# Kernel optimization log

Measured on AMD Instinct MI355X. Metric: run time of the kernel, lower is better.

Reference implementation:

```python
import jax, jax.numpy as jnp
import numpy as np

N_NODES = 50000
N_EDGES = 800000
IN_C, HID_C, OUT_C = 64, 128, 40


def setup_inputs() -> dict:
    key = jax.random.key(0)
    ks = jax.random.split(key, 8)
    x = jax.random.normal(ks[0], (N_NODES, IN_C), dtype=jnp.float32)
    edge_index = jax.random.randint(ks[1], (2, N_EDGES), 0, N_NODES, dtype=jnp.int64)
    def lin(k, fan_in, fan_out):
        # torch Linear default init: U(-1/sqrt(fan_in), 1/sqrt(fan_in))
        bound = 1.0 / np.sqrt(fan_in)
        kw, kb = jax.random.split(k)
        w = jax.random.uniform(kw, (fan_in, fan_out), minval=-bound, maxval=bound, dtype=jnp.float32)
        b = jax.random.uniform(kb, (fan_out,), minval=-bound, maxval=bound, dtype=jnp.float32)
        return w, b
    w1a, b1a = lin(ks[2], IN_C, HID_C)
    w1b, b1b = lin(ks[3], HID_C, HID_C)
    w2a, b2a = lin(ks[4], HID_C, HID_C)
    w2b, b2b = lin(ks[5], HID_C, OUT_C)
    return {
        'x': x, 'edge_index': edge_index,
        'w1a': w1a, 'b1a': b1a, 'w1b': w1b, 'b1b': b1b, 'eps1': jnp.float32(0.0),
        'w2a': w2a, 'b2a': b2a, 'w2b': w2b, 'b2b': b2b, 'eps2': jnp.float32(0.0),
    }


def _gin_conv(x, src, dst, eps, wa, ba, wb, bb):
    # aggregate: sum of neighbor (source) features at each destination node
    agg = jax.ops.segment_sum(x[src], dst, num_segments=N_NODES)  # [N, d]
    h = (1.0 + eps) * x + agg
    h = jax.nn.relu(h @ wa + ba)
    return h @ wb + bb


def reference(x, edge_index, w1a, b1a, w1b, b1b, eps1, w2a, b2a, w2b, b2b, eps2):
    src, dst = edge_index[0], edge_index[1]
    h = _gin_conv(x, src, dst, eps1, w1a, b1a, w1b, b1b)
    h = jax.nn.relu(h)
    # F.dropout(training=False) -> identity at inference
    h = _gin_conv(h, src, dst, eps2, w2a, b2a, w2b, b2b)
    return jax.nn.log_softmax(h, axis=1)
```

## Files before the change

### kernel.cpp

```cpp
#include <hip/hip_runtime.h>
#include <math.h>

#define N_NODES 50000
#define N_EDGES 800000

typedef __attribute__((ext_vector_type(4))) _Float16 half4;
typedef __attribute__((ext_vector_type(8))) _Float16 half8;
typedef __attribute__((ext_vector_type(4))) float f32x4;

__global__ __launch_bounds__(256) void convert_zero(const float4* __restrict__ in,
    half4* __restrict__ out, int* __restrict__ zbase)
{
    int i = blockIdx.x * 256 + threadIdx.x;
    if (i < 450000) zbase[i] = 0;
    if (i < 800000) {
        float4 v = in[i];
        half4 h;
        h[0] = (_Float16)v.x; h[1] = (_Float16)v.y;
        h[2] = (_Float16)v.z; h[3] = (_Float16)v.w;
        out[i] = h;
    }
}

__global__ __launch_bounds__(256) void scatter_ell(const int* __restrict__ src,
    const int* __restrict__ dst, int* __restrict__ cursor8, int* __restrict__ ovcur,
    unsigned short* __restrict__ ellp, unsigned short* __restrict__ ovell)
{
    int g = blockIdx.x & 7;
    int el = (blockIdx.x >> 3) * 256 + threadIdx.x;
    if (el >= 100000) return;
    int e = g * 100000 + el;
    int d = dst[e];
    unsigned short s = (unsigned short)src[e];
    int slot = atomicAdd(&cursor8[g * 50000 + d], 1);
    if (slot < 8) ellp[(size_t)(g * 50000 + d) * 8 + slot] = s;
    else {
        int o = atomicAdd(&ovcur[d], 1);
        if (o < 16) ovell[d * 16 + o] = s;
    }
}

__global__ __launch_bounds__(256) void compact_ell(const int* __restrict__ cursor8,
    const int* __restrict__ ovcur, const unsigned short* __restrict__ ellp,
    const unsigned short* __restrict__ ovell,
    unsigned short* __restrict__ ell, int* __restrict__ deg)
{
    __shared__ unsigned short buf[4][80];
    const int w = threadIdx.x >> 6, lane = threadIdx.x & 63;
    const int node = blockIdx.x * 4 + w;
    const int g = lane >> 3, sl = lane & 7;
    int cg = min(cursor8[g * 50000 + node], 8);
    bool valid = sl < cg;
    unsigned short v = ellp[(size_t)(g * 50000 + node) * 8 + sl];
    unsigned long long mask = __ballot(valid);
    int total = __popcll(mask);
    int pos = __popcll(mask & ((1ULL << lane) - 1ULL));
    if (valid) buf[w][pos] = v;
    int ov = min(ovcur[node], 16);
    if (lane < ov) buf[w][total + lane] = ovell[node * 16 + lane];
    __syncthreads();
    int tot = min(total + ov, 64);
    ell[((size_t)node << 6) + lane] = (lane < tot) ? buf[w][lane] : (unsigned short)0;
    if (lane == 0) deg[node] = tot;
}

__global__ __launch_bounds__(256) void gather64(const half4* __restrict__ rows,
    const unsigned short* __restrict__ ell, const int* __restrict__ deg,
    const float* __restrict__ epsp, half4* __restrict__ z)
{
    const float eps = 1.0f + epsp[0];
    const int lane = threadIdx.x & 63;
    const int q = lane & 15, p = lane >> 4;
    const int wid = blockIdx.x * 4 + (threadIdx.x >> 6);
    const int wstep = gridDim.x * 4;

    for (int node = wid; node < N_NODES; node += wstep) {
        const int cnt = min(deg[node], 64);
        int eidx = (lane < cnt) ? ell[((size_t)node << 6) + lane] : 0;
        float4 acc = make_float4(0.f, 0.f, 0.f, 0.f);
        for (int i = 0; i < cnt; i += 16) {
            int s0 = __shfl(eidx, i + p);
            int s1 = __shfl(eidx, i + 4 + p);
            int s2 = __shfl(eidx, i + 8 + p);
            int s3 = __shfl(eidx, i + 12 + p);
            half4 v0 = rows[s0 * 16 + q];
            half4 v1 = rows[s1 * 16 + q];
            half4 v2 = rows[s2 * 16 + q];
            half4 v3 = rows[s3 * 16 + q];
            bool k0 = (i + p) < cnt, k1 = (i + 4 + p) < cnt;
            bool k2 = (i + 8 + p) < cnt, k3 = (i + 12 + p) < cnt;
            acc.x += (k0?(float)v0[0]:0.f)+(k1?(float)v1[0]:0.f)+(k2?(float)v2[0]:0.f)+(k3?(float)v3[0]:0.f);
            acc.y += (k0?(float)v0[1]:0.f)+(k1?(float)v1[1]:0.f)+(k2?(float)v2[1]:0.f)+(k3?(float)v3[1]:0.f);
            acc.z += (k0?(float)v0[2]:0.f)+(k1?(float)v1[2]:0.f)+(k2?(float)v2[2]:0.f)+(k3?(float)v3[2]:0.f);
            acc.w += (k0?(float)v0[3]:0.f)+(k1?(float)v1[3]:0.f)+(k2?(float)v2[3]:0.f)+(k3?(float)v3[3]:0.f);
        }
        acc.x += __shfl_xor(acc.x, 16); acc.y += __shfl_xor(acc.y, 16);
        acc.z += __shfl_xor(acc.z, 16); acc.w += __shfl_xor(acc.w, 16);
        acc.x += __shfl_xor(acc.x, 32); acc.y += __shfl_xor(acc.y, 32);
        acc.z += __shfl_xor(acc.z, 32); acc.w += __shfl_xor(acc.w, 32);
        if (p == 0) {
            half4 sv = rows[node * 16 + q];
            half4 o;
            o[0] = (_Float16)fmaf(eps, (float)sv[0], acc.x);
            o[1] = (_Float16)fmaf(eps, (float)sv[1], acc.y);
            o[2] = (_Float16)fmaf(eps, (float)sv[2], acc.z);
            o[3] = (_Float16)fmaf(eps, (float)sv[3], acc.w);
            z[node * 16 + q] = o;
        }
    }
}

__global__ __launch_bounds__(256) void gather128(const half4* __restrict__ rows,
    const unsigned short* __restrict__ ell, const int* __restrict__ deg,
    const float* __restrict__ epsp, half4* __restrict__ z)
{
    const float eps = 1.0f + epsp[0];
    const int lane = threadIdx.x & 63;
    const int q = lane & 31, p = lane >> 5;
    const int wid = blockIdx.x * 4 + (threadIdx.x >> 6);
    const int wstep = gridDim.x * 4;

    for (int node = wid; node < N_NODES; node += wstep) {
        const int cnt = min(deg[node], 64);
        int eidx = (lane < cnt) ? ell[((size_t)node << 6) + lane] : 0;
        float4 acc = make_float4(0.f, 0.f, 0.f, 0.f);
        for (int i = 0; i < cnt; i += 8) {
            int s0 = __shfl(eidx, i + p);
            int s1 = __shfl(eidx, i + 2 + p);
            int s2 = __shfl(eidx, i + 4 + p);
            int s3 = __shfl(eidx, i + 6 + p);
            half4 v0 = rows[s0 * 32 + q];
            half4 v1 = rows[s1 * 32 + q];
            half4 v2 = rows[s2 * 32 + q];
            half4 v3 = rows[s3 * 32 + q];
            bool k0 = (i + p) < cnt, k1 = (i + 2 + p) < cnt;
            bool k2 = (i + 4 + p) < cnt, k3 = (i + 6 + p) < cnt;
            acc.x += (k0?(float)v0[0]:0.f)+(k1?(float)v1[0]:0.f)+(k2?(float)v2[0]:0.f)+(k3?(float)v3[0]:0.f);
            acc.y += (k0?(float)v0[1]:0.f)+(k1?(float)v1[1]:0.f)+(k2?(float)v2[1]:0.f)+(k3?(float)v3[1]:0.f);
            acc.z += (k0?(float)v0[2]:0.f)+(k1?(float)v1[2]:0.f)+(k2?(float)v2[2]:0.f)+(k3?(float)v3[2]:0.f);
            acc.w += (k0?(float)v0[3]:0.f)+(k1?(float)v1[3]:0.f)+(k2?(float)v2[3]:0.f)+(k3?(float)v3[3]:0.f);
        }
        acc.x += __shfl_xor(acc.x, 32); acc.y += __shfl_xor(acc.y, 32);
        acc.z += __shfl_xor(acc.z, 32); acc.w += __shfl_xor(acc.w, 32);
        if (p == 0) {
            half4 sv = rows[node * 32 + q];
            half4 o;
            o[0] = (_Float16)fmaf(eps, (float)sv[0], acc.x);
            o[1] = (_Float16)fmaf(eps, (float)sv[1], acc.y);
            o[2] = (_Float16)fmaf(eps, (float)sv[2], acc.z);
            o[3] = (_Float16)fmaf(eps, (float)sv[3], acc.w);
            z[node * 32 + q] = o;
        }
    }
}

template<int KA, int NB, int EPI>
__global__ __launch_bounds__(512) void fused_mlp(const _Float16* __restrict__ A,
    const float* __restrict__ wA, const float* __restrict__ bA,
    const float* __restrict__ wB, const float* __restrict__ bB,
    void* __restrict__ Cout, int NwB)
{
    constexpr int SA = KA / 32, CTB = NB / 16;
    extern __shared__ char smem[];
    half8* fragA = (half8*)smem;
    half8* fragB = (half8*)(smem + SA * 8 * 2 * 64 * 16);
    char* midbase = smem + SA * 8 * 2 * 64 * 16 + 4 * CTB * 2 * 64 * 16;
    const int tid = threadIdx.x;

    for (int idx = tid; idx < SA * 8 * 64; idx += 512) {
        int l = idx & 63, f = idx >> 6;
        int s = f >> 3, ct = f & 7;
        int c = ct * 16 + (l & 15);
        int k0 = s * 32 + (l >> 4) * 8;
        half8 hi, lo;
        #pragma unroll
        for (int i = 0; i < 8; ++i) {
            float wv = wA[(k0 + i) * 128 + c];
            _Float16 h = (_Float16)wv;
            hi[i] = h;
            lo[i] = (_Float16)(wv - (float)h);
        }
        fragA[(f * 2 + 0) * 64 + l] = hi;
        fragA[(f * 2 + 1) * 64 + l] = lo;
    }
    for (int idx = tid; idx < 4 * CTB * 64; idx += 512) {
        int l = idx & 63, f = idx >> 6;
        int s = f / CTB, ct = f % CTB;
        int c = ct * 16 + (l & 15);
        int k0 = s * 32 + (l >> 4) * 8;
        half8 hi, lo;
        #pragma unroll
        for (int i = 0; i < 8; ++i) {
            float wv = (c < NwB) ? wB[(k0 + i) * NwB + c] : 0.0f;
            _Float16 h = (_Float16)wv;
            hi[i] = h;
            lo[i] = (_Float16)(wv - (float)h);
        }
        fragB[(f * 2 + 0) * 64 + l] = hi;
        fragB[(f * 2 + 1) * 64 + l] = lo;
    }
    __syncthreads();

    const int lane = tid & 63;
    const int gg = lane >> 4, r16 = lane & 15;
    const int tile = blockIdx.x * 8 + (tid >> 6);
    if (tile >= N_NODES / 16) return;
    char* my = midbase + (tid >> 6) * 4096;

    const _Float16* Ar = A + (size_t)(tile * 16 + r16) * KA;
    f32x4 acc[8];
    #pragma unroll
    for (int ct = 0; ct < 8; ++ct) acc[ct] = (f32x4){0.f, 0.f, 0.f, 0.f};
    #pragma unroll
    for (int s = 0; s < SA; ++s) {
        half8 a = *(const half8*)(Ar + s * 32 + gg * 8);
        #pragma unroll
        for (int ct = 0; ct < 8; ++ct) {
            half8 bh = fragA[((s * 8 + ct) * 2 + 0) * 64 + lane];
            half8 bo = fragA[((s * 8 + ct) * 2 + 1) * 64 + lane];
            acc[ct] = __builtin_amdgcn_mfma_f32_16x16x32_f16(a, bh, acc[ct], 0, 0, 0);
            acc[ct] = __builtin_amdgcn_mfma_f32_16x16x32_f16(a, bo, acc[ct], 0, 0, 0);
        }
    }
    #pragma unroll
    for (int ct = 0; ct < 8; ++ct) {
        float bb = bA[ct * 16 + r16];
        #pragma unroll
        for (int r = 0; r < 4; ++r) {
            int row = gg * 4 + r;
            float v = fmaxf(acc[ct][r] + bb, 0.0f);
            int off = (row << 8) + ((ct * 16 + r16) << 1);
            off ^= (row & 7) << 4;
            *(_Float16*)(my + off) = (_Float16)v;
        }
    }

    half8 a2[4];
    #pragma unroll
    for (int s = 0; s < 4; ++s) {
        int off = (r16 << 8) + (s << 6) + (gg << 4);
        off ^= (r16 & 7) << 4;
        a2[s] = *(const half8*)(my + off);
    }
    f32x4 acc2[CTB];
    #pragma unroll
    for (int ct = 0; ct < CTB; ++ct) acc2[ct] = (f32x4){0.f, 0.f, 0.f, 0.f};
    #pragma unroll
    for (int s = 0; s < 4; ++s) {
        #pragma unroll
        for (int ct = 0; ct < CTB; ++ct) {
            half8 bh = fragB[((s * CTB + ct) * 2 + 0) * 64 + lane];
            half8 bo = fragB[((s * CTB + ct) * 2 + 1) * 64 + lane];
            acc2[ct] = __builtin_amdgcn_mfma_f32_16x16x32_f16(a2[s], bh, acc2[ct], 0, 0, 0);
            acc2[ct] = __builtin_amdgcn_mfma_f32_16x16x32_f16(a2[s], bo, acc2[ct], 0, 0, 0);
        }
    }

    if (EPI == 0) {
        _Float16* C = (_Float16*)Cout;
        #pragma unroll
        for (int ct = 0; ct < CTB; ++ct) {
            float bb = bB[ct * 16 + r16];
            #pragma unroll
            for (int r = 0; r < 4; ++r) {
                int row = tile * 16 + gg * 4 + r;
                float v = fmaxf(acc2[ct][r] + bb, 0.0f);
                C[(size_t)row * NB + ct * 16 + r16] = (_Float16)v;
            }
        }
    } else {
        float* C = (float*)Cout;
        const bool va2 = r16 < 8;
        float bl0 = bB[r16], bl1 = bB[16 + r16];
        float bl2 = va2 ? bB[32 + r16] : 0.0f;
        #pragma unroll
        for (int r = 0; r < 4; ++r) {
            int row = tile * 16 + gg * 4 + r;
            float v0 = acc2[0][r] + bl0;
            float v1 = acc2[1][r] + bl1;
            float v2 = acc2[2][r] + bl2;
            float mx = fmaxf(fmaxf(v0, v1), va2 ? v2 : -__builtin_inff());
            mx = fmaxf(mx, __shfl_xor(mx, 1));
            mx = fmaxf(mx, __shfl_xor(mx, 2));
            mx = fmaxf(mx, __shfl_xor(mx, 4));
            mx = fmaxf(mx, __shfl_xor(mx, 8));
            float sm = expf(v0 - mx) + expf(v1 - mx) + (va2 ? expf(v2 - mx) : 0.f);
            sm += __shfl_xor(sm, 1);
            sm += __shfl_xor(sm, 2);
            sm += __shfl_xor(sm, 4);
            sm += __shfl_xor(sm, 8);
            float ls = logf(sm) + mx;
            C[row * 40 + r16] = v0 - ls;
            C[row * 40 + 16 + r16] = v1 - ls;
            if (va2) C[row * 40 + 32 + r16] = v2 - ls;
        }
    }
}

extern "C" void kernel_launch(void* const* d_in, const int* in_sizes, int n_in,
                              void* d_out, int out_size, void* d_ws, size_t ws_size,
                              hipStream_t stream) {
    const float* x    = (const float*)d_in[0];
    const int*   ei   = (const int*)d_in[1];
    const float* w1a  = (const float*)d_in[2];
    const float* b1a  = (const float*)d_in[3];
    const float* w1b  = (const float*)d_in[4];
    const float* b1b  = (const float*)d_in[5];
    const float* eps1 = (const float*)d_in[6];
    const float* w2a  = (const float*)d_in[7];
    const float* b2a  = (const float*)d_in[8];
    const float* w2b  = (const float*)d_in[9];
    const float* b2b  = (const float*)d_in[10];
    const float* eps2 = (const float*)d_in[11];
    float* out = (float*)d_out;

    const int* srcIdx = ei;
    const int* dstIdx = ei + N_EDGES;

    char* ws = (char*)d_ws;
    int*            cursor8 = (int*)(ws);
    int*            ovcur   = (int*)(ws + 1600000);
    unsigned short* ellp    = (unsigned short*)(ws + 1800000);
    unsigned short* ovell   = (unsigned short*)(ws + 8200000);
    unsigned short* ell     = (unsigned short*)(ws + 9800000);
    int*            deg     = (int*)(ws + 16200000);
    _Float16*       xh      = (_Float16*)(ws + 16400000);
    _Float16*       z1h     = (_Float16*)(ws + 22800000);
    _Float16*       h1h     = (_Float16*)(ws + 29200000);
    _Float16*       z2h     = (_Float16*)(ws + 42000000);

    convert_zero<<<3125, 256, 0, stream>>>((const float4*)x, (half4*)xh, cursor8);
    scatter_ell<<<3128, 256, 0, stream>>>(srcIdx, dstIdx, cursor8, ovcur, ellp, ovell);
    compact_ell<<<12500, 256, 0, stream>>>(cursor8, ovcur, ellp, ovell, ell, deg);

    gather64<<<2048, 256, 0, stream>>>((const half4*)xh, ell, deg, eps1, (half4*)z1h);
    fused_mlp<64, 128, 0><<<391, 512, 131072, stream>>>(z1h, w1a, b1a, w1b, b1b, h1h, 128);
    gather128<<<2048, 256, 0, stream>>>((const half4*)h1h, ell, deg, eps2, (half4*)z2h);
    fused_mlp<128, 48, 1><<<391, 512, 122880, stream>>>(z2h, w2a, b2a, w2b, b2b, out, 40);
}
```

Baseline: 215.4 us.

## Fuse ELL compaction into first gather, pad with zero dummy row, widen loads

Merges the compact_ell kernel into the first-layer gather, so each wave builds its node's neighbor list in LDS and immediately aggregates from it. This removes one launch and one re-read of the ELL array. Empty ELL slots now point to a zero-filled dummy row (node 50000) in both feature buffers, which drops the per-neighbor bounds predicates. Both gathers switch from half4 to half8 loads with 8-wide accumulators. The cost is extra workspace offsets and zero-initialisation, and gather64c no longer has a __syncthreads before reading the LDS buffer; it relies on wave-level LDS ordering instead.

```diff
diff --git a/kernel.cpp b/kernel.cpp
--- a/kernel.cpp
+++ b/kernel.cpp
@@ -3,13 +3,14 @@
 
 #define N_NODES 50000
 #define N_EDGES 800000
+#define DUMMY   50000
 
 typedef __attribute__((ext_vector_type(4))) _Float16 half4;
 typedef __attribute__((ext_vector_type(8))) _Float16 half8;
 typedef __attribute__((ext_vector_type(4))) float f32x4;
 
 __global__ __launch_bounds__(256) void convert_zero(const float4* __restrict__ in,
-    half4* __restrict__ out, int* __restrict__ zbase)
+    half4* __restrict__ xh4, int* __restrict__ zbase, half4* __restrict__ h1dummy)
 {
     int i = blockIdx.x * 256 + threadIdx.x;
     if (i < 450000) zbase[i] = 0;
@@ -18,7 +19,14 @@
         half4 h;
         h[0] = (_Float16)v.x; h[1] = (_Float16)v.y;
         h[2] = (_Float16)v.z; h[3] = (_Float16)v.w;
-        out[i] = h;
+        xh4[i] = h;
+    } else if (i < 800016) {
+        half4 zer = {(_Float16)0.f, (_Float16)0.f, (_Float16)0.f, (_Float16)0.f};
+        xh4[i] = zer;
+    }
+    if (i < 32) {
+        half4 zer = {(_Float16)0.f, (_Float16)0.f, (_Float16)0.f, (_Float16)0.f};
+        h1dummy[i] = zer;
     }
 }
 
@@ -40,33 +48,71 @@
     }
 }
 
-__global__ __launch_bounds__(256) void compact_ell(const int* __restrict__ cursor8,
-    const int* __restrict__ ovcur, const unsigned short* __restrict__ ellp,
-    const unsigned short* __restrict__ ovell,
-    unsigned short* __restrict__ ell, int* __restrict__ deg)
+__global__ __launch_bounds__(256) void gather64c(const half8* __restrict__ rows,
+    const int* __restrict__ cursor8, const int* __restrict__ ovcur,
+    const unsigned short* __restrict__ ellp, const unsigned short* __restrict__ ovell,
+    unsigned short* __restrict__ ell, int* __restrict__ deg,
+    const float* __restrict__ epsp, half8* __restrict__ z)
 {
     __shared__ unsigned short buf[4][80];
-    const int w = threadIdx.x >> 6, lane = threadIdx.x & 63;
-    const int node = blockIdx.x * 4 + w;
-    const int g = lane >> 3, sl = lane & 7;
-    int cg = min(cursor8[g * 50000 + node], 8);
-    bool valid = sl < cg;
-    unsigned short v = ellp[(size_t)(g * 50000 + node) * 8 + sl];
-    unsigned long long mask = __ballot(valid);
-    int total = __popcll(mask);
-    int pos = __popcll(mask & ((1ULL << lane) - 1ULL));
-    if (valid) buf[w][pos] = v;
-    int ov = min(ovcur[node], 16);
-    if (lane < ov) buf[w][total + lane] = ovell[node * 16 + lane];
-    __syncthreads();
-    int tot = min(total + ov, 64);
-    ell[((size_t)node << 6) + lane] = (lane < tot) ? buf[w][lane] : (unsigned short)0;
-    if (lane == 0) deg[node] = tot;
-}
-
-__global__ __launch_bounds__(256) void gather64(const half4* __restrict__ rows,
+    const float eps = 1.0f + epsp[0];
+    const int lane = threadIdx.x & 63;
+    const int w = threadIdx.x >> 6;
+    const int q = lane & 7, p = lane >> 3;
+    const int sl = lane & 7;
+    const int wid = blockIdx.x * 4 + w;
+    const int wstep = gridDim.x * 4;
+
+    for (int node = wid; node < N_NODES; node += wstep) {
+        int cg = min(cursor8[p * 50000 + node], 8);
+        bool valid = sl < cg;
+        unsigned short v = ellp[(size_t)(p * 50000 + node) * 8 + sl];
+        unsigned long long mask = __ballot(valid);
+        int total = __popcll(mask);
+        int pos = __popcll(mask & ((1ULL << lane) - 1ULL));
+        if (valid) buf[w][pos] = v;
+        int ov = min(ovcur[node], 16);
+        if (lane < ov) buf[w][total + lane] = ovell[node * 16 + lane];
+        int tot = min(total + ov, 64);
+        unsigned short e = (lane < tot) ? buf[w][lane] : (unsigned short)DUMMY;
+        ell[((size_t)node << 6) + lane] = e;
+        if (lane == 0) deg[node] = tot;
+        int eidx = e;
+        float acc[8];
+        #pragma unroll
+        for (int j = 0; j < 8; ++j) acc[j] = 0.f;
+        for (int i = 0; i < tot; i += 32) {
+            int s0 = __shfl(eidx, i + p);
+            int s1 = __shfl(eidx, i + 8 + p);
+            int s2 = __shfl(eidx, i + 16 + p);
+            int s3 = __shfl(eidx, i + 24 + p);
+            half8 v0 = rows[s0 * 8 + q];
+            half8 v1 = rows[s1 * 8 + q];
+            half8 v2 = rows[s2 * 8 + q];
+            half8 v3 = rows[s3 * 8 + q];
+            #pragma unroll
+            for (int j = 0; j < 8; ++j)
+                acc[j] += ((float)v0[j] + (float)v1[j]) + ((float)v2[j] + (float)v3[j]);
+        }
+        #pragma unroll
+        for (int j = 0; j < 8; ++j) {
+            acc[j] += __shfl_xor(acc[j], 8);
+            acc[j] += __shfl_xor(acc[j], 16);
+            acc[j] += __shfl_xor(acc[j], 32);
+        }
+        if (p == 0) {
+            half8 sv = rows[node * 8 + q];
+            half8 o;
+            #pragma unroll
+            for (int j = 0; j < 8; ++j) o[j] = (_Float16)fmaf(eps, (float)sv[j], acc[j]);
+            z[node * 8 + q] = o;
+        }
+    }
+}
+
+__global__ __launch_bounds__(256) void gather128(const half8* __restrict__ rows,
     const unsigned short* __restrict__ ell, const int* __restrict__ deg,
-    const float* __restrict__ epsp, half4* __restrict__ z)
+    const float* __restrict__ epsp, half8* __restrict__ z)
 {
     const float eps = 1.0f + epsp[0];
     const int lane = threadIdx.x & 63;
@@ -75,81 +121,35 @@
     const int wstep = gridDim.x * 4;
 
     for (int node = wid; node < N_NODES; node += wstep) {
-        const int cnt = min(deg[node], 64);
-        int eidx = (lane < cnt) ? ell[((size_t)node << 6) + lane] : 0;
-        float4 acc = make_float4(0.f, 0.f, 0.f, 0.f);
+        const int cnt = deg[node];
+        int eidx = ell[((size_t)node << 6) + lane];
+        float acc[8];
+        #pragma unroll
+        for (int j = 0; j < 8; ++j) acc[j] = 0.f;
         for (int i = 0; i < cnt; i += 16) {
             int s0 = __shfl(eidx, i + p);
             int s1 = __shfl(eidx, i + 4 + p);
             int s2 = __shfl(eidx, i + 8 + p);
             int s3 = __shfl(eidx, i + 12 + p);
-            half4 v0 = rows[s0 * 16 + q];
-            half4 v1 = rows[s1 * 16 + q];
-            half4 v2 = rows[s2 * 16 + q];
-            half4 v3 = rows[s3 * 16 + q];
-            bool k0 = (i + p) < cnt, k1 = (i + 4 + p) < cnt;
-            bool k2 = (i + 8 + p) < cnt, k3 = (i + 12 + p) < cnt;
-            acc.x += (k0?(float)v0[0]:0.f)+(k1?(float)v1[0]:0.f)+(k2?(float)v2[0]:0.f)+(k3?(float)v3[0]:0.f);
-            acc.y += (k0?(float)v0[1]:0.f)+(k1?(float)v1[1]:0.f)+(k2?(float)v2[1]:0.f)+(k3?(float)v3[1]:0.f);
-            acc.z += (k0?(float)v0[2]:0.f)+(k1?(float)v1[2]:0.f)+(k2?(float)v2[2]:0.f)+(k3?(float)v3[2]:0.f);
-            acc.w += (k0?(float)v0[3]:0.f)+(k1?(float)v1[3]:0.f)+(k2?(float)v2[3]:0.f)+(k3?(float)v3[3]:0.f);
-        }
-        acc.x += __shfl_xor(acc.x, 16); acc.y += __shfl_xor(acc.y, 16);
-        acc.z += __shfl_xor(acc.z, 16); acc.w += __shfl_xor(acc.w, 16);
-        acc.x += __shfl_xor(acc.x, 32); acc.y += __shfl_xor(acc.y, 32);
-        acc.z += __shfl_xor(acc.z, 32); acc.w += __shfl_xor(acc.w, 32);
+            half8 v0 = rows[s0 * 16 + q];
+            half8 v1 = rows[s1 * 16 + q];
+            half8 v2 = rows[s2 * 16 + q];
+            half8 v3 = rows[s3 * 16 + q];
+            #pragma unroll
+            for (int j = 0; j < 8; ++j)
+                acc[j] += ((float)v0[j] + (float)v1[j]) + ((float)v2[j] + (float)v3[j]);
+        }
+        #pragma unroll
+        for (int j = 0; j < 8; ++j) {
+            acc[j] += __shfl_xor(acc[j], 16);
+            acc[j] += __shfl_xor(acc[j], 32);
+        }
         if (p == 0) {
-            half4 sv = rows[node * 16 + q];
-            half4 o;
-            o[0] = (_Float16)fmaf(eps, (float)sv[0], acc.x);
-            o[1] = (_Float16)fmaf(eps, (float)sv[1], acc.y);
-            o[2] = (_Float16)fmaf(eps, (float)sv[2], acc.z);
-            o[3] = (_Float16)fmaf(eps, (float)sv[3], acc.w);
+            half8 sv = rows[node * 16 + q];
+            half8 o;
+            #pragma unroll
+            for (int j = 0; j < 8; ++j) o[j] = (_Float16)fmaf(eps, (float)sv[j], acc[j]);
             z[node * 16 + q] = o;
-        }
-    }
-}
-
-__global__ __launch_bounds__(256) void gather128(const half4* __restrict__ rows,
-    const unsigned short* __restrict__ ell, const int* __restrict__ deg,
-    const float* __restrict__ epsp, half4* __restrict__ z)
-{
-    const float eps = 1.0f + epsp[0];
-    const int lane = threadIdx.x & 63;
-    const int q = lane & 31, p = lane >> 5;
-    const int wid = blockIdx.x * 4 + (threadIdx.x >> 6);
-    const int wstep = gridDim.x * 4;
-
-    for (int node = wid; node < N_NODES; node += wstep) {
-        const int cnt = min(deg[node], 64);
-        int eidx = (lane < cnt) ? ell[((size_t)node << 6) + lane] : 0;
-        float4 acc = make_float4(0.f, 0.f, 0.f, 0.f);
-        for (int i = 0; i < cnt; i += 8) {
-            int s0 = __shfl(eidx, i + p);
-            int s1 = __shfl(eidx, i + 2 + p);
-            int s2 = __shfl(eidx, i + 4 + p);
-            int s3 = __shfl(eidx, i + 6 + p);
-            half4 v0 = rows[s0 * 32 + q];
-            half4 v1 = rows[s1 * 32 + q];
-            half4 v2 = rows[s2 * 32 + q];
-            half4 v3 = rows[s3 * 32 + q];
-            bool k0 = (i + p) < cnt, k1 = (i + 2 + p) < cnt;
-            bool k2 = (i + 4 + p) < cnt, k3 = (i + 6 + p) < cnt;
-            acc.x += (k0?(float)v0[0]:0.f)+(k1?(float)v1[0]:0.f)+(k2?(float)v2[0]:0.f)+(k3?(float)v3[0]:0.f);
-            acc.y += (k0?(float)v0[1]:0.f)+(k1?(float)v1[1]:0.f)+(k2?(float)v2[1]:0.f)+(k3?(float)v3[1]:0.f);
-            acc.z += (k0?(float)v0[2]:0.f)+(k1?(float)v1[2]:0.f)+(k2?(float)v2[2]:0.f)+(k3?(float)v3[2]:0.f);
-            acc.w += (k0?(float)v0[3]:0.f)+(k1?(float)v1[3]:0.f)+(k2?(float)v2[3]:0.f)+(k3?(float)v3[3]:0.f);
-        }
-        acc.x += __shfl_xor(acc.x, 32); acc.y += __shfl_xor(acc.y, 32);
-        acc.z += __shfl_xor(acc.z, 32); acc.w += __shfl_xor(acc.w, 32);
-        if (p == 0) {
-            half4 sv = rows[node * 32 + q];
-            half4 o;
-            o[0] = (_Float16)fmaf(eps, (float)sv[0], acc.x);
-            o[1] = (_Float16)fmaf(eps, (float)sv[1], acc.y);
-            o[2] = (_Float16)fmaf(eps, (float)sv[2], acc.z);
-            o[3] = (_Float16)fmaf(eps, (float)sv[3], acc.w);
-            z[node * 32 + q] = o;
         }
     }
 }
@@ -325,16 +325,17 @@
     unsigned short* ell     = (unsigned short*)(ws + 9800000);
     int*            deg     = (int*)(ws + 16200000);
     _Float16*       xh      = (_Float16*)(ws + 16400000);
-    _Float16*       z1h     = (_Float16*)(ws + 22800000);
-    _Float16*       h1h     = (_Float16*)(ws + 29200000);
-    _Float16*       z2h     = (_Float16*)(ws + 42000000);
-
-    convert_zero<<<3125, 256, 0, stream>>>((const float4*)x, (half4*)xh, cursor8);
+    _Float16*       z1h     = (_Float16*)(ws + 22800128);
+    _Float16*       h1h     = (_Float16*)(ws + 29200128);
+    _Float16*       z2h     = (_Float16*)(ws + 42000384);
+    half4*          h1dummy = (half4*)(h1h + (size_t)DUMMY * 128);
+
+    convert_zero<<<3126, 256, 0, stream>>>((const float4*)x, (half4*)xh, cursor8, h1dummy);
     scatter_ell<<<3128, 256, 0, stream>>>(srcIdx, dstIdx, cursor8, ovcur, ellp, ovell);
-    compact_ell<<<12500, 256, 0, stream>>>(cursor8, ovcur, ellp, ovell, ell, deg);
-
-    gather64<<<2048, 256, 0, stream>>>((const half4*)xh, ell, deg, eps1, (half4*)z1h);
+
+    gather64c<<<2048, 256, 0, stream>>>((const half8*)xh, cursor8, ovcur, ellp, ovell,
+                                        ell, deg, eps1, (half8*)z1h);
     fused_mlp<64, 128, 0><<<391, 512, 131072, stream>>>(z1h, w1a, b1a, w1b, b1b, h1h, 128);
-    gather128<<<2048, 256, 0, stream>>>((const half4*)h1h, ell, deg, eps2, (half4*)z2h);
+    gather128<<<2048, 256, 0, stream>>>((const half8*)h1h, ell, deg, eps2, (half8*)z2h);
     fused_mlp<128, 48, 1><<<391, 512, 122880, stream>>>(z2h, w2a, b2a, w2b, b2b, out, 40);
 }
```

Result: faster. 207.6 us (-3.6%).
